# Performance work log

Hardware: AMD Instinct MI355X
Metric: run time of the kernel (lower is better)

The kernel has to match this reference:

```python
import jax, jax.numpy as jnp
import numpy as np

W_PROFILE, W_PLANFORM, W_MEAN = 0.5, 0.3, 0.2
CELL_SIZE = 10.0
EPS = 1e-08


def _kernels():
    sobel_x = np.array([[-1, 0, 1], [-2, 0, 2], [-1, 0, 1]], np.float32) / 8.0
    sobel_y = np.array([[-1, -2, -1], [0, 0, 0], [1, 2, 1]], np.float32) / 8.0
    k_xx = np.array([[1, -2, 1], [1, -2, 1], [1, -2, 1]], np.float32) / 3.0
    k_yy = np.array([[1, 1, 1], [-2, -2, -2], [1, 1, 1]], np.float32) / 3.0
    k_xy = np.array([[-1, 0, 1], [0, 0, 0], [1, 0, -1]], np.float32) / 4.0
    # stack into one [5,1,3,3] OIHW kernel -> single fused conv for all 5 stencils
    return jnp.asarray(np.stack([sobel_x, sobel_y, k_xx, k_xy, k_yy])[:, None])

_K = _kernels()


def _curvatures(dem):
    # dem: [B,1,H,W] -> derivatives p,q,r,s,t each [B,1,H,W]
    d = jax.lax.conv_general_dilated(dem, _K, window_strides=(1, 1), padding='SAME',
                                     dimension_numbers=('NCHW', 'OIHW', 'NCHW'))
    p = d[:, 0:1] / CELL_SIZE
    q = d[:, 1:2] / CELL_SIZE
    r = d[:, 2:3] / CELL_SIZE ** 2
    s = d[:, 3:4] / CELL_SIZE ** 2
    t = d[:, 4:5] / CELL_SIZE ** 2
    p2, q2, pq = p * p, q * q, p * q
    denom1 = p2 + q2
    denom2 = (1 + denom1) ** 1.5
    profile = (r * p2 + 2 * s * pq + t * q2) / (denom1 * jnp.sqrt(1 + denom1) + EPS)
    planform = (r * q2 - 2 * s * pq + t * p2) / (denom1 ** 1.5 + EPS)
    mean = ((1 + q2) * r - 2 * pq * s + (1 + p2) * t) / (2 * denom2 + EPS)
    flat = denom1 < EPS
    profile = jnp.where(flat, 0.0, profile)
    planform = jnp.where(flat, 0.0, planform)
    return profile, planform, mean


def setup_inputs() -> dict:
    key = jax.random.key(0)
    k1, k2 = jax.random.split(key)
    shape = (16, 1, 1024, 1024)
    return {
        'pred': jax.random.normal(k1, shape, dtype=jnp.float32),
        'target': jax.random.normal(k2, shape, dtype=jnp.float32),
    }


def reference(pred, target):
    pp, pl, pm = _curvatures(pred)
    tp, tl, tm = _curvatures(target)
    loss_profile = jnp.mean(jnp.abs(pp - tp))
    loss_planform = jnp.mean(jnp.abs(pl - tl))
    loss_mean = jnp.mean(jnp.abs(pm - tm))
    return W_PROFILE * loss_profile + W_PLANFORM * loss_planform + W_MEAN * loss_mean
```

## Files before the change

kernel.cpp:

```cpp
#include <hip/hip_runtime.h>
#include <math.h>


constexpr int IMG_B = 16;
constexpr int IMG_H = 1024;
constexpr int IMG_W = 1024;
constexpr int ROWS  = 16;
constexpr int BLOCK = 256;
constexpr int TILES_X = IMG_W / BLOCK;
constexpr int TILES_Y = IMG_H / ROWS;
constexpr int NBLOCKS = IMG_B * TILES_Y * TILES_X;
constexpr float EPS = 1e-8f;

constexpr float A2 = 1.0f / 6400.0f;
constexpr float Bc = 1.0f / 300.0f;
constexpr float C2 = 1.0f / 200.0f;

typedef float f2v __attribute__((ext_vector_type(2)));

__device__ __forceinline__ f2v pk_fma(f2v a, f2v b, f2v c) {
    return __builtin_elementwise_fma(a, b, c);
}

struct Rowv { f2v hx, hs, rs; };

__device__ __forceinline__ void curv_pair(const Rowv& a, const Rowv& b, const Rowv& c,
                                          f2v& prof, f2v& plan, f2v& mean2)
{
    const f2v A2f = {A2, A2}, Bcf = {Bc, Bc}, C2f = {C2, C2};
    const f2v m3  = {-3.0f, -3.0f}, two = {2.0f, 2.0f};
    const f2v epsf = {EPS, EPS};

    const f2v gx  = pk_fma(two, b.hx, a.hx + c.hx);
    const f2v gy  = c.hs - a.hs;
    const f2v tot = (a.rs + c.rs) + b.rs;
    const f2v H   = (a.hs + c.hs) + b.hs;
    const f2v rxx = pk_fma(m3, H - tot, tot);
    const f2v tyy = pk_fma(m3, b.rs, tot);
    const f2v sxy = a.hx - c.hx;

    const f2v gx2 = gx * gx, gy2 = gy * gy, gxgy = gx * gy;
    const f2v g2  = gx2 + gy2;
    const f2v d1  = A2f * g2;
    const f2v od  = d1 + f2v{1.0f, 1.0f};

    f2v rsq_od, sq_d1;
    rsq_od.x = __builtin_amdgcn_rsqf(od.x);
    rsq_od.y = __builtin_amdgcn_rsqf(od.y);
    sq_d1.x  = __builtin_amdgcn_sqrtf(d1.x);
    sq_d1.y  = __builtin_amdgcn_sqrtf(d1.y);
    const f2v sq_od = od * rsq_od;

    const f2v h1    = pk_fma(tyy, gy2, rxx * gx2);
    const f2v h3    = pk_fma(tyy, gx2, rxx * gy2);
    const f2v h2c   = C2f * (sxy * gxgy);
    const f2v nprof = A2f * pk_fma(Bcf, h1,  h2c);
    const f2v nplan = A2f * pk_fma(Bcf, h3, -h2c);
    const f2v mnum  = pk_fma(Bcf, rxx + tyy, nplan);

    const f2v den_p = pk_fma(d1, sq_od, epsf);
    const f2v den_l = pk_fma(d1, sq_d1, epsf);
    const f2v plprod = den_p * den_l;
    f2v rcpPL;
    rcpPL.x = __builtin_amdgcn_rcpf(plprod.x);
    rcpPL.y = __builtin_amdgcn_rcpf(plprod.y);

    prof  = (nprof * den_l) * rcpPL;
    plan  = (nplan * den_p) * rcpPL;
    mean2 = mnum * ((rsq_od * rsq_od) * rsq_od);
    prof.x = (d1.x < EPS) ? 0.0f : prof.x;
    prof.y = (d1.y < EPS) ? 0.0f : prof.y;
    plan.x = (d1.x < EPS) ? 0.0f : plan.x;
    plan.y = (d1.y < EPS) ? 0.0f : plan.y;
}

__global__ __launch_bounds__(BLOCK) void curv_loss_main(
    const float* __restrict__ pred, const float* __restrict__ targ,
    float* __restrict__ blocksums)
{
    const int tid = threadIdx.x;
    const int b   = blockIdx.x;
    const int tx  = b & (TILES_X - 1);
    const int ty  = (b >> 2) & (TILES_Y - 1);
    const int img = b >> 8;
    const int y0  = ty * ROWS;
    const int x   = tx * BLOCK + tid;

    const size_t ibase = (size_t)img * (size_t)(IMG_H * IMG_W);
    const char* __restrict__ Pc = (const char*)(pred + ibase);
    const char* __restrict__ Tc = (const char*)(targ + ibase);

    const bool xm = (x > 0);
    const bool xp = (x < IMG_W - 1);
    const int eL = (x + (xm ? -1 : 0)) << 2;
    const int eC = x << 2;
    const int eR = (x + (xp ? +1 : 0)) << 2;

    auto prep = [&](int y, Rowv& o) {
        if ((unsigned)y < (unsigned)IMG_H) {
            const int vo = y << 12;
            const float pl = *(const float*)(Pc + vo + eL);
            const float tl = *(const float*)(Tc + vo + eL);
            const float pc = *(const float*)(Pc + vo + eC);
            const float tc = *(const float*)(Tc + vo + eC);
            const float pr = *(const float*)(Pc + vo + eR);
            const float tr = *(const float*)(Tc + vo + eR);
            const f2v w0 = {xm ? pl : 0.0f, xm ? tl : 0.0f};
            const f2v w1 = {pc, tc};
            const f2v w2 = {xp ? pr : 0.0f, xp ? tr : 0.0f};
            const f2v e = w0 + w2;
            o.hx = w2 - w0;
            o.hs = pk_fma(f2v{2.0f, 2.0f}, w1, e);
            o.rs = e + w1;
        } else {
            o.hx = f2v{0.0f, 0.0f}; o.hs = f2v{0.0f, 0.0f}; o.rs = f2v{0.0f, 0.0f};
        }
    };

    Rowv w[3];
    prep(y0 - 1, w[0]);
    prep(y0,     w[1]);

    float acc = 0.0f;
#pragma unroll
    for (int i = 0; i < ROWS; ++i) {
        const int ia = i % 3, ib = (i + 1) % 3, ic = (i + 2) % 3;
        prep(y0 + i + 1, w[ic]);
        f2v prof, plan, mean2;
        curv_pair(w[ia], w[ib], w[ic], prof, plan, mean2);
        acc = fmaf(0.5f, fabsf(prof.x  - prof.y),  acc);
        acc = fmaf(0.3f, fabsf(plan.x  - plan.y),  acc);
        acc = fmaf(0.1f, fabsf(mean2.x - mean2.y), acc);
    }

#pragma unroll
    for (int off = 32; off > 0; off >>= 1) acc += __shfl_down(acc, off, 64);
    __shared__ float ws[BLOCK / 64];
    const int lane = tid & 63, wid = tid >> 6;
    if (lane == 0) ws[wid] = acc;
    __syncthreads();
    if (tid == 0)
        blocksums[b] = (ws[0] + ws[1]) + (ws[2] + ws[3]);
}

__global__ __launch_bounds__(BLOCK) void curv_loss_final(
    const float* __restrict__ blocksums, float* __restrict__ out)
{
    const int tid = threadIdx.x;
    float v = 0.0f;
#pragma unroll
    for (int i = 0; i < NBLOCKS / BLOCK; ++i) v += blocksums[i * BLOCK + tid];
#pragma unroll
    for (int off = 32; off > 0; off >>= 1) v += __shfl_down(v, off, 64);
    __shared__ float ws[BLOCK / 64];
    const int lane = tid & 63, wid = tid >> 6;
    if (lane == 0) ws[wid] = v;
    __syncthreads();
    if (tid == 0) {
        const float tot = (ws[0] + ws[1]) + (ws[2] + ws[3]);
        out[0] = tot * (1.0f / (float)(IMG_B * IMG_H * IMG_W));
    }
}

extern "C" void kernel_launch(void* const* d_in, const int* in_sizes, int n_in,
                              void* d_out, int out_size, void* d_ws, size_t ws_size,
                              hipStream_t stream)
{
    const float* pred = (const float*)d_in[0];
    const float* targ = (const float*)d_in[1];
    float* out = (float*)d_out;
    float* blocksums = (float*)d_ws;

    curv_loss_main<<<NBLOCKS, BLOCK, 0, stream>>>(pred, targ, blocksums);
    curv_loss_final<<<1, BLOCK, 0, stream>>>(blocksums, out);
}
```

Measured before the change: 153.5 us.

## Stage input tile with halo in LDS before computing stencil curvatures

The kernel now loads an (ROWS+2) x (BLOCK+2) tile of interleaved pred/target pairs into shared memory once, with two threads fetching the right halo columns. The stencil then reads its left, centre and right neighbours from LDS instead of issuing three global loads per row per tensor. This cuts redundant global and L1 traffic from horizontally overlapping loads. In exchange it adds about 37 KB of LDS per block, which may lower occupancy, plus a barrier that prevents overlapping loads with compute.

```diff
diff --git a/kernel.cpp b/kernel.cpp
--- a/kernel.cpp
+++ b/kernel.cpp
@@ -84,48 +84,61 @@
     const int ty  = (b >> 2) & (TILES_Y - 1);
     const int img = b >> 8;
     const int y0  = ty * ROWS;
-    const int x   = tx * BLOCK + tid;
+    const int x0  = tx * BLOCK;
+    const int x   = x0 + tid;
 
     const size_t ibase = (size_t)img * (size_t)(IMG_H * IMG_W);
-    const char* __restrict__ Pc = (const char*)(pred + ibase);
-    const char* __restrict__ Tc = (const char*)(targ + ibase);
+    const float* __restrict__ P = pred + ibase;
+    const float* __restrict__ T = targ + ibase;
 
-    const bool xm = (x > 0);
-    const bool xp = (x < IMG_W - 1);
-    const int eL = (x + (xm ? -1 : 0)) << 2;
-    const int eC = x << 2;
-    const int eR = (x + (xp ? +1 : 0)) << 2;
+    __shared__ f2v S[ROWS + 2][BLOCK + 2];
+    __shared__ float ws[BLOCK / 64];
 
-    auto prep = [&](int y, Rowv& o) {
-        if ((unsigned)y < (unsigned)IMG_H) {
-            const int vo = y << 12;
-            const float pl = *(const float*)(Pc + vo + eL);
-            const float tl = *(const float*)(Tc + vo + eL);
-            const float pc = *(const float*)(Pc + vo + eC);
-            const float tc = *(const float*)(Tc + vo + eC);
-            const float pr = *(const float*)(Pc + vo + eR);
-            const float tr = *(const float*)(Tc + vo + eR);
-            const f2v w0 = {xm ? pl : 0.0f, xm ? tl : 0.0f};
-            const f2v w1 = {pc, tc};
-            const f2v w2 = {xp ? pr : 0.0f, xp ? tr : 0.0f};
-            const f2v e = w0 + w2;
-            o.hx = w2 - w0;
-            o.hs = pk_fma(f2v{2.0f, 2.0f}, w1, e);
-            o.rs = e + w1;
+    const bool m1  = (x > 0);
+    const int  gc1 = m1 ? (x - 1) : 0;
+    const int  c2   = (tid == 0) ? BLOCK : ((tid == 64) ? (BLOCK + 1) : -1);
+    const int  gx2r = x0 + 255 + ((tid == 64) ? 1 : 0);
+    const bool m2   = (gx2r < IMG_W);
+    const int  gc2  = m2 ? gx2r : (IMG_W - 1);
+
+#pragma unroll
+    for (int r = 0; r < ROWS + 2; ++r) {
+        const int yr = y0 - 1 + r;
+        if ((unsigned)yr < (unsigned)IMG_H) {
+            const float* Pr = P + ((size_t)yr << 10);
+            const float* Tr = T + ((size_t)yr << 10);
+            const float p1 = Pr[gc1], t1 = Tr[gc1];
+            S[r][tid] = f2v{m1 ? p1 : 0.0f, m1 ? t1 : 0.0f};
+            if (c2 >= 0) {
+                const float p2 = Pr[gc2], t2 = Tr[gc2];
+                S[r][c2] = f2v{m2 ? p2 : 0.0f, m2 ? t2 : 0.0f};
+            }
         } else {
-            o.hx = f2v{0.0f, 0.0f}; o.hs = f2v{0.0f, 0.0f}; o.rs = f2v{0.0f, 0.0f};
+            S[r][tid] = f2v{0.0f, 0.0f};
+            if (c2 >= 0) S[r][c2] = f2v{0.0f, 0.0f};
         }
+    }
+    __syncthreads();
+
+    auto lds_prep = [&](int r, Rowv& o) {
+        const f2v w0 = S[r][tid];
+        const f2v w1 = S[r][tid + 1];
+        const f2v w2 = S[r][tid + 2];
+        const f2v e = w0 + w2;
+        o.hx = w2 - w0;
+        o.hs = pk_fma(f2v{2.0f, 2.0f}, w1, e);
+        o.rs = e + w1;
     };
 
     Rowv w[3];
-    prep(y0 - 1, w[0]);
-    prep(y0,     w[1]);
+    lds_prep(0, w[0]);
+    lds_prep(1, w[1]);
 
     float acc = 0.0f;
 #pragma unroll
     for (int i = 0; i < ROWS; ++i) {
         const int ia = i % 3, ib = (i + 1) % 3, ic = (i + 2) % 3;
-        prep(y0 + i + 1, w[ic]);
+        lds_prep(i + 2, w[ic]);
         f2v prof, plan, mean2;
         curv_pair(w[ia], w[ib], w[ic], prof, plan, mean2);
         acc = fmaf(0.5f, fabsf(prof.x  - prof.y),  acc);
@@ -135,7 +148,6 @@
 
 #pragma unroll
     for (int off = 32; off > 0; off >>= 1) acc += __shfl_down(acc, off, 64);
-    __shared__ float ws[BLOCK / 64];
     const int lane = tid & 63, wid = tid >> 6;
     if (lane == 0) ws[wid] = acc;
     __syncthreads();
```

Measured after the change: 206.4 us. 1.34x slower.
